# Performance work log

Measured on AMD Instinct MI355X. Metric: run time of the kernel, lower is better.

Reference implementation:

```python
import jax, jax.numpy as jnp
import numpy as np

WS = 8          # window_size
OWS = 12        # overlap_win_size = int(8*0.5)+8
PAD = 2         # (OWS-WS)//2
HEADS = 6
DH = 16         # dim_head
INNER = HEADS * DH  # 96
SCALE = DH ** -0.5


def rel_to_abs(x):
    # x: (b, l, m) with m = 2*r - 1
    b, l, m = x.shape
    r = (m + 1) // 2
    x = jnp.concatenate([x, jnp.zeros((b, l, 1), x.dtype)], axis=2)
    flat = x.reshape(b, l * (m + 1))
    flat = jnp.concatenate([flat, jnp.zeros((b, m - l), x.dtype)], axis=1)
    final = flat.reshape(b, l + 1, m)[:, :l, m - r:]
    return final  # (b, l, r)


def relative_logits_1d(q, rel_k):
    # q: (B, X, Y, d), rel_k: (2r-1, d)
    B, X, Y, _ = q.shape
    r = (rel_k.shape[0] + 1) // 2
    logits = jnp.einsum('bxyd,rd->bxyr', q, rel_k)           # (B, X, Y, 2r-1)
    logits = rel_to_abs(logits.reshape(B * X, Y, -1)).reshape(B, X, Y, r)
    logits = jnp.broadcast_to(logits[:, :, None], (B, X, r, Y, r))  # b x i y j
    return logits


def rel_pos_emb(q, rel_height, rel_width):
    # q: (B, WS*WS, d) -> bias (B, WS*WS, OWS*OWS)
    B, _, d = q.shape
    qg = q.reshape(B, WS, WS, d)
    lw = relative_logits_1d(qg, rel_width)                   # (B, x, i, y, j)
    lw = lw.transpose(0, 1, 3, 2, 4).reshape(B, WS * WS, OWS * OWS)  # b (x y) (i j)
    lh = relative_logits_1d(qg.transpose(0, 2, 1, 3), rel_height)    # (B, y, i, x, j) roles swapped
    lh = lh.transpose(0, 3, 1, 4, 2).reshape(B, WS * WS, OWS * OWS)  # b (y x) (j i)
    return lw + lh


def unfold_windows(t, nh, nw):
    # torch nn.Unfold(kernel=OWS, stride=WS, padding=PAD) then
    # rearrange 'b (c j) i -> (b i) j c' -> (b*nh*nw, OWS*OWS, C)
    b, C, _, _ = t.shape
    tp = jnp.pad(t, ((0, 0), (0, 0), (PAD, PAD), (PAD, PAD)))
    ridx = (jnp.arange(nh) * WS)[:, None] + jnp.arange(OWS)   # (nh, OWS)
    cidx = (jnp.arange(nw) * WS)[:, None] + jnp.arange(OWS)   # (nw, OWS)
    p = tp[:, :, ridx, :]            # (b, C, nh, OWS, Wp)
    p = p[:, :, :, :, cidx]          # (b, C, nh, OWS, nw, OWS)
    p = p.transpose(0, 2, 4, 3, 5, 1)  # (b, nh, nw, OWS, OWS, C)
    return p.reshape(b * nh * nw, OWS * OWS, C)


def split_heads(t):
    # (B, n, heads*dh) -> (B*heads, n, dh)
    B, n, _ = t.shape
    return t.reshape(B, n, HEADS, DH).transpose(0, 2, 1, 3).reshape(B * HEADS, n, DH)


def setup_inputs() -> dict:
    key = jax.random.key(0)
    k = jax.random.split(key, 5)
    x = jax.random.normal(k[0], (2, 96, 256, 256), jnp.float32)
    qkv_w = jax.random.normal(k[1], (288, 96), jnp.float32) * 0.05
    qkv_b = jnp.zeros((288,), jnp.float32)
    proj_w = jax.random.normal(k[2], (96, 96), jnp.float32) * 0.05
    proj_b = jnp.zeros((96,), jnp.float32)
    rel_height = jax.random.normal(k[3], (23, 16), jnp.float32) * SCALE
    rel_width = jax.random.normal(k[4], (23, 16), jnp.float32) * SCALE
    return {"x": x, "qkv_w": qkv_w, "qkv_b": qkv_b, "proj_w": proj_w,
            "proj_b": proj_b, "rel_height": rel_height, "rel_width": rel_width}


def reference(x, qkv_w, qkv_b, proj_w, proj_b, rel_height, rel_width):
    b, c, h, w = x.shape
    nh, nw = h // WS, w // WS
    qkv = jnp.einsum('oc,bchw->bohw', qkv_w, x) + qkv_b[None, :, None, None]
    qs, ks, vs = jnp.split(qkv, 3, axis=1)  # each (b, INNER, h, w)
    # queries: non-overlapping windows 'b c (h p1) (w p2) -> (b h w) (p1 p2) c'
    qs = qs.reshape(b, INNER, nh, WS, nw, WS).transpose(0, 2, 4, 3, 5, 1)
    qs = qs.reshape(b * nh * nw, WS * WS, INNER)
    ks = unfold_windows(ks, nh, nw)  # (b*nh*nw, OWS*OWS, INNER)
    vs = unfold_windows(vs, nh, nw)
    qs, ks, vs = map(split_heads, (qs, ks, vs))  # (B*heads, n, DH)
    qs = qs * SCALE
    attn = jnp.einsum('bqd,bkd->bqk', qs, ks)
    attn = attn + rel_pos_emb(qs, rel_height, rel_width)
    attn = jax.nn.softmax(attn, axis=-1)
    out = jnp.einsum('bqk,bkd->bqd', attn, vs)  # (b*nh*nw*heads, WS*WS, DH)
    out = out.reshape(b, nh, nw, HEADS, WS, WS, DH)
    out = out.transpose(0, 3, 6, 1, 4, 2, 5).reshape(b, INNER, h, w)
    out = jnp.einsum('oc,bchw->bohw', proj_w, out) + proj_b[None, :, None, None]
    return out
```

## Files before the change

kernel.cpp:

```cpp
#include <hip/hip_runtime.h>
#include <hip/hip_bf16.h>


typedef __attribute__((ext_vector_type(8))) short bf16x8;
typedef __attribute__((ext_vector_type(4))) float f32x4;

__device__ __forceinline__ f32x4 mfma16(bf16x8 a, bf16x8 b, f32x4 c) {
  return __builtin_amdgcn_mfma_f32_16x16x32_bf16(a, b, c, 0, 0, 0);
}
__device__ __forceinline__ short f2b(float f) {
  unsigned u = __builtin_bit_cast(unsigned, f);
  unsigned r = u + 0x7fffu + ((u >> 16) & 1u);
  return (short)(r >> 16);
}
__device__ __forceinline__ unsigned cvtpk(float lo, float hi) {
  unsigned r;
  asm("v_cvt_pk_bf16_f32 %0, %1, %2" : "=v"(r) : "v"(lo), "v"(hi));
  return r;
}
__device__ __forceinline__ void splitf(float x, short& h, short& l) {
  unsigned u = __builtin_bit_cast(unsigned, x);
  h = (short)(u >> 16);
  float fh = __builtin_bit_cast(float, u & 0xffff0000u);
  l = f2b(x - fh);
}

#define KPLANE 1081600L
#define QS (0.25f * 1.44269504f)

__global__ __launch_bounds__(256) void prep_kernel(
    const float* __restrict__ qkv_w, const float* __restrict__ proj_w,
    const float* __restrict__ rel_h, const float* __restrict__ rel_w,
    const float* __restrict__ qkv_b,
    short* __restrict__ qwh, short* __restrict__ qwl,
    short* __restrict__ pwh, short* __restrict__ pwl,
    short* __restrict__ rhb, short* __restrict__ rwb,
    float* __restrict__ sbias, short* __restrict__ k_t) {
  int i = blockIdx.x * 256 + threadIdx.x;
  if (i < 288 * 96) {
    float wv = qkv_w[i];
    if (i < 96 * 96) wv *= QS;
    short h, l;
    splitf(wv, h, l);
    qwh[i] = h;
    qwl[i] = l;
  }
  if (i < 96 * 96) {
    short h, l;
    splitf(proj_w[i], h, l);
    pwh[i] = h;
    pwl[i] = l;
  }
  if (i < 368) {
    rhb[i] = f2b(rel_h[i]);
    rwb[i] = f2b(rel_w[i]);
  }
  if (i < 288) sbias[i] = qkv_b[i] * (i < 96 ? QS : 1.0f);
  if (i < 12 * 2064) {
    int plane = i / 2064, r = i - plane * 2064;
    int py, px;
    if (r < 1040) {
      int rowid = r / 260;
      py = (rowid < 2) ? rowid : 256 + rowid;
      px = r - rowid * 260;
    } else {
      int r2 = r - 1040;
      py = 2 + (r2 >> 2);
      int cid = r2 & 3;
      px = (cid < 2) ? cid : 256 + cid;
    }
    bf16x8 z = {0, 0, 0, 0, 0, 0, 0, 0};
    long base = (long)plane * KPLANE + (long)(py * 260 + px) * 16;
    *(bf16x8*)(k_t + base) = z;
    *(bf16x8*)(k_t + base + 8) = z;
  }
}

__global__ __launch_bounds__(256) void qkv_kernel(
    const float* __restrict__ x, const short* __restrict__ qwh,
    const short* __restrict__ qwl, const float* __restrict__ sbias,
    short* __restrict__ q_t, short* __restrict__ k_t,
    short* __restrict__ v_t) {
  const int tid = threadIdx.x;
  const int wave = tid >> 6, lane = tid & 63;
  const int quad = lane >> 4, col = lane & 15;
  const int blk = blockIdx.x;
  const int b = blk >> 8, row = blk & 255;

  const float* xw = x + (((long)b * 96) << 16) + row * 256 + wave * 64 + col;
  bf16x8 bx[4][3];
#pragma unroll
  for (int tile = 0; tile < 4; ++tile)
#pragma unroll
    for (int ks = 0; ks < 3; ++ks) {
      const float* p = xw + tile * 16 + (((long)(ks * 32 + quad * 8)) << 16);
      float v0 = p[0];
      float v1 = p[1L << 16];
      float v2 = p[2L << 16];
      float v3 = p[3L << 16];
      float v4 = p[4L << 16];
      float v5 = p[5L << 16];
      float v6 = p[6L << 16];
      float v7 = p[7L << 16];
      union { unsigned u[4]; bf16x8 w; } t;
      t.u[0] = cvtpk(v0, v1);
      t.u[1] = cvtpk(v2, v3);
      t.u[2] = cvtpk(v4, v5);
      t.u[3] = cvtpk(v6, v7);
      bx[tile][ks] = t.w;
    }

  const short* wbh = qwh + col * 96 + quad * 8;
  const short* wbl = qwl + col * 96 + quad * 8;
  bf16x8 wh[3], wl[3];
#pragma unroll
  for (int ks = 0; ks < 3; ++ks) {
    wh[ks] = *(const bf16x8*)(wbh + ks * 32);
    wl[ks] = *(const bf16x8*)(wbl + ks * 32);
  }

  const long pixb = (long)blk * 256 + wave * 64 + col;
  short* kbase = k_t + (long)b * KPLANE +
                 ((long)((row + 2) * 260 + wave * 64 + col + 2)) * 16 +
                 quad * 4;

#pragma unroll
  for (int t6 = 0; t6 < 18; ++t6) {
    bf16x8 nh[3], nl[3];
    if (t6 < 17) {
#pragma unroll
      for (int ks = 0; ks < 3; ++ks) {
        nh[ks] = *(const bf16x8*)(wbh + (t6 + 1) * 1536 + ks * 32);
        nl[ks] = *(const bf16x8*)(wbl + (t6 + 1) * 1536 + ks * 32);
      }
    }
    f32x4 bv = *(const f32x4*)(sbias + t6 * 16 + quad * 4);
    f32x4 acc[4] = {bv, bv, bv, bv};
#pragma unroll
    for (int ks = 0; ks < 3; ++ks)
#pragma unroll
      for (int tile = 0; tile < 4; ++tile) {
        acc[tile] = mfma16(wh[ks], bx[tile][ks], acc[tile]);
        acc[tile] = mfma16(wl[ks], bx[tile][ks], acc[tile]);
      }
#pragma unroll
    for (int tile = 0; tile < 4; ++tile) {
      unsigned d0 = cvtpk(acc[tile][0], acc[tile][1]);
      unsigned d1 = cvtpk(acc[tile][2], acc[tile][3]);
      if (t6 >= 6 && t6 < 12) {
        short* kp = kbase + (long)(t6 - 6) * (2 * KPLANE) + tile * 256;
        *(unsigned*)kp = d0;
        *(unsigned*)(kp + 2) = d1;
      } else {
        short* plane = (t6 < 6 ? q_t : v_t) +
                       (long)(t6 < 6 ? t6 : t6 - 12) * 2097152 + pixb * 16 +
                       tile * 256 + quad * 4;
        *(unsigned*)plane = d0;
        *(unsigned*)(plane + 2) = d1;
      }
    }
    if (t6 < 17) {
#pragma unroll
      for (int ks = 0; ks < 3; ++ks) {
        wh[ks] = nh[ks];
        wl[ks] = nl[ks];
      }
    }
  }
}

__global__ __launch_bounds__(256) void attn_kernel(
    const short* __restrict__ q_t, const short* __restrict__ k_t,
    const short* __restrict__ v_t, const short* __restrict__ rhb,
    const short* __restrict__ rwb, short* __restrict__ ao) {
  __shared__ __attribute__((aligned(16))) short v_lds[16][168];
  __shared__ __attribute__((aligned(16))) char scratch[4][5248];

  const int orig = blockIdx.x, head = blockIdx.y;
  const int win = ((orig & 7) << 8) | (orig >> 3);
  const int b = win >> 10, wy = (win & 1023) >> 5, wx = win & 31;
  const int y0 = wy * 8 - 2, x0 = wx * 8 - 2;
  const long pb = (long)b << 16;
  const int tid = threadIdx.x;

  if (tid < 160) {
    const int key = tid;
    bool valid = false;
    long pix = 0;
    if (key < 144) {
      int kh = key / 12, kw = key - kh * 12;
      int gy = y0 + kh, gx = x0 + kw;
      valid = ((unsigned)gy < 256u) && ((unsigned)gx < 256u);
      pix = pb + gy * 256 + gx;
    }
    if (valid) {
      const short* src = v_t + (long)head * 2097152 + pix * 16;
      union { bf16x8 v; short s[8]; } u0, u1;
      u0.v = *(const bf16x8*)src;
      u1.v = *(const bf16x8*)(src + 8);
      for (int d = 0; d < 8; ++d) {
        v_lds[d][key] = u0.s[d];
        v_lds[d + 8][key] = u1.s[d];
      }
    } else {
      for (int d = 0; d < 16; ++d) v_lds[d][key] = 0;
    }
  }
  __syncthreads();

  const int wave = tid >> 6, lane = tid & 63;
  const int quad = lane >> 4, col = lane & 15;
  float* dWs = (float*)scratch[wave];
  float* dHt = dWs + 600;
  unsigned* ppd = (unsigned*)scratch[wave];

  const short* qp = q_t + (long)head * 2097152;
  const short* kpb = k_t + (long)(head * 2 + b) * KPLANE;

  bf16x8 qf = {0, 0, 0, 0, 0, 0, 0, 0};
  if (quad < 2) {
    int qg = wave * 16 + col;
    int qy = qg >> 3, qx = qg & 7;
    qf = *(const bf16x8*)(qp + (pb + (wy * 8 + qy) * 256 + wx * 8 + qx) * 16 +
                          quad * 8);
  }

  for (int nt = 0; nt < 2; ++nt) {
    int r = nt * 16 + col;
    bf16x8 bw = {0, 0, 0, 0, 0, 0, 0, 0}, bh2 = bw;
    if (quad < 2 && r < 23) {
      bw = *(const bf16x8*)(rwb + r * 16 + quad * 8);
      bh2 = *(const bf16x8*)(rhb + r * 16 + quad * 8);
    }
    f32x4 z = {0.f, 0.f, 0.f, 0.f};
    f32x4 aw = mfma16(qf, bw, z);
    f32x4 ah = mfma16(qf, bh2, z);
    if (r < 23)
      for (int r4 = 0; r4 < 4; ++r4) {
        int ql = quad * 4 + r4;
        dWs[(r + (ql & 7)) * 20 + ql] = aw[r4];
        dHt[r * 20 + ql] = ah[r4];
      }
  }

  f32x4 L[9];
  {
    int kh = (col >= 12) ? 1 : 0, kw = col - 12 * kh;
    const short* ka =
        kpb + (long)((wy * 8 + kh) * 260 + wx * 8 + kw) * 16 + quad * 8;
    for (int nt = 0; nt < 9; ++nt) {
      bf16x8 kf = *(const bf16x8*)ka;
      f32x4 z = {0.f, 0.f, 0.f, 0.f};
      L[nt] = mfma16(qf, kf, z);
      kw += 4;
      if (kw >= 12) {
        kw -= 12;
        ka += 512 * 16;
      } else {
        ka += 264 * 16;
      }
    }
  }

  const int qy4 = wave * 2 + (quad >> 1);
  {
    int kh = (col >= 12) ? 1 : 0, kw = col - 12 * kh;
    for (int nt = 0; nt < 9; ++nt) {
      f32x4 wv = *(const f32x4*)&dWs[(11 + kw) * 20 + quad * 4];
      f32x4 hv = *(const f32x4*)&dHt[(11 + kh - qy4) * 20 + quad * 4];
      for (int r4 = 0; r4 < 4; ++r4)
        L[nt][r4] = __builtin_amdgcn_exp2f(L[nt][r4] + wv[r4] + hv[r4]);
      kw += 4;
      kh += 1;
      if (kw >= 12) {
        kw -= 12;
        kh += 1;
      }
    }
  }
  asm volatile("" ::: "memory");

  for (int nt = 0; nt < 9; ++nt) {
    unsigned d0 = cvtpk(L[nt][0], L[nt][1]);
    unsigned d1 = cvtpk(L[nt][2], L[nt][3]);
    int base = (nt * 16 + col) * 9 + quad * 2;
    ppd[base] = d0;
    ppd[base + 1] = d1;
  }

  const unsigned sel = (col & 1) ? 0x07060302u : 0x05040100u;
  const bf16x8 ones = {0x3F80, 0x3F80, 0x3F80, 0x3F80,
                       0x3F80, 0x3F80, 0x3F80, 0x3F80};
  f32x4 oacc = {0.f, 0.f, 0.f, 0.f}, oaccS = oacc;
  for (int ks = 0; ks < 5; ++ks) {
    int k0 = ks * 32 + quad * 8;
    bool live = k0 < 144;
    int k0c = live ? k0 : 136;
    const unsigned* rp = ppd + k0c * 9 + (col >> 1);
    unsigned r0 = rp[0], r1 = rp[9], r2 = rp[18], r3 = rp[27];
    unsigned r4v = rp[36], r5 = rp[45], r6 = rp[54], r7 = rp[63];
    union { unsigned u[4]; bf16x8 v; } pu;
    pu.u[0] = live ? __builtin_amdgcn_perm(r1, r0, sel) : 0u;
    pu.u[1] = live ? __builtin_amdgcn_perm(r3, r2, sel) : 0u;
    pu.u[2] = live ? __builtin_amdgcn_perm(r5, r4v, sel) : 0u;
    pu.u[3] = live ? __builtin_amdgcn_perm(r7, r6, sel) : 0u;
    bf16x8 vb = *(const bf16x8*)&v_lds[col][ks * 32 + quad * 8];
    oacc = mfma16(pu.v, vb, oacc);
    oaccS = mfma16(pu.v, ones, oaccS);
  }
  for (int r4 = 0; r4 < 4; ++r4) {
    int qg = wave * 16 + quad * 4 + r4;
    int qy = qg >> 3, qx = qg & 7;
    float val = oacc[r4] * __builtin_amdgcn_rcpf(oaccS[r4]);
    ao[(long)head * 2097152 +
       (pb + (wy * 8 + qy) * 256 + wx * 8 + qx) * 16 + col] = f2b(val);
  }
}

__global__ __launch_bounds__(256) void proj_kernel(
    const short* __restrict__ ao, const short* __restrict__ pwh,
    const short* __restrict__ pwl, const float* __restrict__ bias,
    float* __restrict__ out) {
  const int tid = threadIdx.x;
  const int wave = tid >> 6, lane = tid & 63;
  const int quad = lane >> 4, col = lane & 15;
  const int blk = blockIdx.x;
  const int b = blk >> 8;
  const long pix0 = (long)blk * 256 + wave * 64 + col;

  bf16x8 bfr[4][3];
#pragma unroll
  for (int tile = 0; tile < 4; ++tile)
#pragma unroll
    for (int ks = 0; ks < 3; ++ks) {
      int head = 2 * ks + (quad >> 1);
      bfr[tile][ks] =
          *(const bf16x8*)(ao + (long)head * 2097152 +
                           (pix0 + tile * 16) * 16 + (quad & 1) * 8);
    }

  const short* wbh = pwh + col * 96 + quad * 8;
  const short* wbl = pwl + col * 96 + quad * 8;
  bf16x8 ah[3], al[3];
#pragma unroll
  for (int ks = 0; ks < 3; ++ks) {
    ah[ks] = *(const bf16x8*)(wbh + ks * 32);
    al[ks] = *(const bf16x8*)(wbl + ks * 32);
  }
  float* ob = out + (((long)(b * 96 + quad * 4)) << 16) + (blk & 255) * 256 +
              wave * 64 + col;
#pragma unroll
  for (int mt = 0; mt < 6; ++mt) {
    bf16x8 nh[3], nl[3];
    if (mt < 5) {
#pragma unroll
      for (int ks = 0; ks < 3; ++ks) {
        nh[ks] = *(const bf16x8*)(wbh + (mt + 1) * 1536 + ks * 32);
        nl[ks] = *(const bf16x8*)(wbl + (mt + 1) * 1536 + ks * 32);
      }
    }
    f32x4 bv = *(const f32x4*)(bias + mt * 16 + quad * 4);
    f32x4 acc[4] = {bv, bv, bv, bv};
#pragma unroll
    for (int ks = 0; ks < 3; ++ks)
#pragma unroll
      for (int tile = 0; tile < 4; ++tile) {
        acc[tile] = mfma16(ah[ks], bfr[tile][ks], acc[tile]);
        acc[tile] = mfma16(al[ks], bfr[tile][ks], acc[tile]);
      }
    float* obm = ob + ((long)(mt * 16) << 16);
#pragma unroll
    for (int tile = 0; tile < 4; ++tile)
#pragma unroll
      for (int r = 0; r < 4; ++r)
        obm[((long)r << 16) + tile * 16] = acc[tile][r];
    if (mt < 5) {
#pragma unroll
      for (int ks = 0; ks < 3; ++ks) {
        ah[ks] = nh[ks];
        al[ks] = nl[ks];
      }
    }
  }
}

extern "C" void kernel_launch(void* const* d_in, const int* in_sizes, int n_in,
                              void* d_out, int out_size, void* d_ws,
                              size_t ws_size, hipStream_t stream) {
  const float* x = (const float*)d_in[0];
  const float* qkv_w = (const float*)d_in[1];
  const float* qkv_b = (const float*)d_in[2];
  const float* proj_w = (const float*)d_in[3];
  const float* proj_b = (const float*)d_in[4];
  const float* rel_h = (const float*)d_in[5];
  const float* rel_w = (const float*)d_in[6];

  const long NPIXC = 131072L * 96L;
  short* q_t = (short*)d_ws;
  short* k_t = q_t + NPIXC;
  short* v_t = k_t + 12 * KPLANE;
  short* ao = v_t + NPIXC;
  short* qwh = ao + NPIXC;
  short* qwl = qwh + 288 * 96;
  short* pwh = qwl + 288 * 96;
  short* pwl = pwh + 96 * 96;
  short* rhb = pwl + 96 * 96;
  short* rwb = rhb + 368;
  float* sbias = (float*)(rwb + 368);
  float* out = (float*)d_out;

  hipLaunchKernelGGL(prep_kernel, dim3(108), dim3(256), 0, stream, qkv_w,
                     proj_w, rel_h, rel_w, qkv_b, qwh, qwl, pwh, pwl, rhb, rwb,
                     sbias, k_t);
  hipLaunchKernelGGL(qkv_kernel, dim3(512), dim3(256), 0, stream, x, qwh, qwl,
                     sbias, q_t, k_t, v_t);
  hipLaunchKernelGGL(attn_kernel, dim3(2048, 6), dim3(256), 0, stream, q_t,
                     k_t, v_t, rhb, rwb, ao);
  hipLaunchKernelGGL(proj_kernel, dim3(512), dim3(256), 0, stream, ao, pwh,
                     pwl, proj_b, out);
}
```

Measured before the change: 195.8 us.

## Restructure QK tiles per key row and fold rel-pos bias into MFMA accumulator

The QK^T step now uses one MFMA tile per key row: 12 tiles whose columns hold 12 keys each, with 4 lanes idle. Previously it used 9 tiles that packed 144 keys densely. Because each column is a fixed key-width position, the width bias becomes a single register load, and the height bias is one load per row. Both are added into the MFMA accumulator as its initial value, so the separate bias-add loop goes away. The cost is 12 MFMAs instead of 9 and masked stores, traded for fewer LDS reads and simpler indexing.

```diff
diff --git a/kernel.cpp b/kernel.cpp
--- a/kernel.cpp
+++ b/kernel.cpp
@@ -242,51 +242,55 @@
         dHt[r * 20 + ql] = ah[r4];
       }
   }
-
-  f32x4 L[9];
-  {
-    int kh = (col >= 12) ? 1 : 0, kw = col - 12 * kh;
-    const short* ka =
-        kpb + (long)((wy * 8 + kh) * 260 + wx * 8 + kw) * 16 + quad * 8;
-    for (int nt = 0; nt < 9; ++nt) {
-      bf16x8 kf = *(const bf16x8*)ka;
-      f32x4 z = {0.f, 0.f, 0.f, 0.f};
-      L[nt] = mfma16(qf, kf, z);
-      kw += 4;
-      if (kw >= 12) {
-        kw -= 12;
-        ka += 512 * 16;
-      } else {
-        ka += 264 * 16;
-      }
-    }
-  }
-
+  asm volatile("" ::: "memory");
+
+  const f32x4 wv = *(const f32x4*)&dWs[(11 + col) * 20 + quad * 4];
   const int qy4 = wave * 2 + (quad >> 1);
-  {
-    int kh = (col >= 12) ? 1 : 0, kw = col - 12 * kh;
-    for (int nt = 0; nt < 9; ++nt) {
-      f32x4 wv = *(const f32x4*)&dWs[(11 + kw) * 20 + quad * 4];
-      f32x4 hv = *(const f32x4*)&dHt[(11 + kh - qy4) * 20 + quad * 4];
-      for (int r4 = 0; r4 < 4; ++r4)
-        L[nt][r4] = __builtin_amdgcn_exp2f(L[nt][r4] + wv[r4] + hv[r4]);
-      kw += 4;
-      kh += 1;
-      if (kw >= 12) {
-        kw -= 12;
-        kh += 1;
-      }
-    }
-  }
+  f32x4 hva[6];
+#pragma unroll
+  for (int nt = 0; nt < 6; ++nt)
+    hva[nt] = *(const f32x4*)&dHt[(11 + nt - qy4) * 20 + quad * 4];
   asm volatile("" ::: "memory");
 
-  for (int nt = 0; nt < 9; ++nt) {
-    unsigned d0 = cvtpk(L[nt][0], L[nt][1]);
-    unsigned d1 = cvtpk(L[nt][2], L[nt][3]);
-    int base = (nt * 16 + col) * 9 + quad * 2;
-    ppd[base] = d0;
-    ppd[base + 1] = d1;
-  }
+  const short* kb =
+      kpb + (long)((wy * 8) * 260 + wx * 8 + col) * 16 + quad * 8;
+  unsigned* wp0 = ppd + col * 9 + quad * 2;
+
+#pragma unroll
+  for (int nt = 0; nt < 6; ++nt) {
+    bf16x8 kf = *(const bf16x8*)(kb + (long)nt * 4160);
+    f32x4 acc = wv + hva[nt];
+    f32x4 L = mfma16(qf, kf, acc);
+    unsigned d0 = cvtpk(__builtin_amdgcn_exp2f(L[0]),
+                        __builtin_amdgcn_exp2f(L[1]));
+    unsigned d1 = cvtpk(__builtin_amdgcn_exp2f(L[2]),
+                        __builtin_amdgcn_exp2f(L[3]));
+    if (col < 12) {
+      wp0[nt * 108] = d0;
+      wp0[nt * 108 + 1] = d1;
+    }
+  }
+  asm volatile("" ::: "memory");
+  f32x4 hvb[6];
+#pragma unroll
+  for (int nt = 0; nt < 6; ++nt)
+    hvb[nt] = *(const f32x4*)&dHt[(17 + nt - qy4) * 20 + quad * 4];
+  asm volatile("" ::: "memory");
+#pragma unroll
+  for (int nt = 0; nt < 6; ++nt) {
+    bf16x8 kf = *(const bf16x8*)(kb + (long)(nt + 6) * 4160);
+    f32x4 acc = wv + hvb[nt];
+    f32x4 L = mfma16(qf, kf, acc);
+    unsigned d0 = cvtpk(__builtin_amdgcn_exp2f(L[0]),
+                        __builtin_amdgcn_exp2f(L[1]));
+    unsigned d1 = cvtpk(__builtin_amdgcn_exp2f(L[2]),
+                        __builtin_amdgcn_exp2f(L[3]));
+    if (col < 12) {
+      wp0[(nt + 6) * 108] = d0;
+      wp0[(nt + 6) * 108 + 1] = d1;
+    }
+  }
+  asm volatile("" ::: "memory");
 
   const unsigned sel = (col & 1) ? 0x07060302u : 0x05040100u;
   const bf16x8 ones = {0x3F80, 0x3F80, 0x3F80, 0x3F80,
```

New measurement: 203.8 us. 1.04x slower.
